# Kernel optimization log

Measured on AMD Instinct MI355X. Metric: run time of the kernel, lower is better.

The kernel has to match this reference:

```python
import jax, jax.numpy as jnp
import numpy as np

GAMMA = 0.997
N_STEPS = 5
EPS = 1e-3
Q_WEIGHTS = np.array([1.0, 0.5, 0.0, 2.0], dtype=np.float32)


def _rescale(x):
    # sign(x) * (sqrt(|x|+1) - 1) + eps * x
    return jnp.sign(x) * (jnp.sqrt(jnp.abs(x) + 1.0) - 1.0) + EPS * x


def _inv_rescale(x):
    sign = jnp.sign(x)
    sqrt_arg = 1.0 + 4.0 * EPS * (jnp.abs(x) + 1.0 + EPS)
    square = ((jnp.sqrt(sqrt_arg) - 1.0) / (2.0 * EPS)) ** 2
    return sign * (square - 1.0)


def setup_inputs() -> dict:
    key = jax.random.key(0)
    ks = jax.random.split(key, 6)
    B, T, Q = 4096, 512, 4
    current_q_value = jax.random.normal(ks[0], (B, T, Q), dtype=jnp.float32)
    next_q_value = jax.random.normal(ks[1], (B, T, Q), dtype=jnp.float32)
    log_p = jax.random.normal(ks[2], (B, T), dtype=jnp.float32)
    reward = jax.random.normal(ks[3], (B, T, Q), dtype=jnp.float32)
    is_done = jax.random.bernoulli(ks[4], 0.02, (B, T)).astype(jnp.float32)
    mask = jax.random.bernoulli(ks[5], 0.95, (B, T)).astype(jnp.float32)
    return {
        "current_q_value": current_q_value,
        "next_q_value": next_q_value,
        "log_p": log_p,
        "reward": reward,
        "is_done": is_done,
        "mask": mask,
    }


def reference(current_q_value, next_q_value, log_p, reward, is_done, mask):
    B, T, Q = reward.shape
    q_w = jnp.asarray(Q_WEIGHTS)[None, None, :]                     # (1,1,Q)
    nz = (q_w != 0)
    inv_qw = jnp.where(nz, 1.0 / jnp.where(nz, q_w, 1.0), 0.0)      # (1,1,Q)
    inv_num_q = 1.0 / float((Q_WEIGHTS != 0).sum())

    m = mask[..., None]                                             # (B,T,1)
    d = is_done[..., None]                                          # (B,T,1)

    nq = m * (1.0 - d) * _inv_rescale(next_q_value)                 # (B,T,Q)
    lp = inv_num_q * inv_qw * (m * (1.0 - d) * log_p[..., None])    # (B,T,Q)

    pad = jnp.zeros((B, N_STEPS - 1, Q), dtype=reward.dtype)
    pad_reward = jnp.concatenate([m * reward, pad], axis=1)         # (B,T+n-1,Q)
    lp_pad = jnp.concatenate([lp, pad], axis=1)                     # (B,T+n-1,Q)

    gpow = GAMMA ** jnp.arange(N_STEPS, dtype=jnp.float32)          # gamma^0..gamma^{n-1}
    widx = jnp.arange(T)[:, None] + jnp.arange(N_STEPS)[None, :]    # (T,n) window indices

    reward_sum = jnp.einsum('btnq,n->btq', pad_reward[:, widx, :], gpow)
    log_p_sum = jnp.einsum('btnq,n->btq', lp_pad[:, widx, :], gpow * GAMMA)

    idxs = jnp.minimum(T - 1, jnp.arange(T) + N_STEPS - 1)          # (T,)
    # NOTE: original code uses gamma**idx (absolute index), reproduced faithfully
    next_term = (GAMMA ** idxs.astype(jnp.float32))[None, :, None] * nq[:, idxs, :]

    target = _rescale(reward_sum + next_term + log_p_sum)           # (B,T,Q)
    loss = 0.5 * m * q_w * (current_q_value - target) ** 2
    return loss
```

## Files before the change

### kernel.cpp

```cpp
#include <hip/hip_runtime.h>
#include <math.h>

#define T_DIM 512
#define GAMMA_F 0.997f
#define EPS_F 1e-3f
#define LOG2_GAMMA (-0.0043345907f)

typedef float v4f __attribute__((ext_vector_type(4)));

__device__ __forceinline__ float inv_rescale_f(float x) {
    float s = (x > 0.f) ? 1.f : ((x < 0.f) ? -1.f : 0.f);
    float sqrt_arg = 1.f + 4.f * EPS_F * (fabsf(x) + 1.f + EPS_F);
    float q = (sqrtf(sqrt_arg) - 1.f) * (1.f / (2.f * EPS_F));
    return s * (q * q - 1.f);
}

__device__ __forceinline__ float rescale_f(float x) {
    return copysignf(sqrtf(fabsf(x) + 1.f) - 1.f, x) + EPS_F * x;
}

__global__ __launch_bounds__(512) void nstep_qloss_kernel(
    const float* __restrict__ cur_q,
    const float* __restrict__ next_q,
    const float* __restrict__ log_p,
    const float* __restrict__ reward,
    const float* __restrict__ is_done,
    const float* __restrict__ mask,
    float* __restrict__ out)
{
    __shared__ v4f   s_mr [T_DIM + 4];
    __shared__ float s_lpv[T_DIM + 4];
    __shared__ float s_md [T_DIM + 4];

    const int t    = threadIdx.x;
    const int base = blockIdx.x * T_DIM;
    const int idx  = base + t;
    const int s4   = (t + 4 < T_DIM) ? t + 4 : T_DIM - 1;

    const v4f* rew4 = (const v4f*)reward;
    const v4f* nq4  = (const v4f*)next_q;
    const v4f* cq4  = (const v4f*)cur_q;
    v4f*       out4 = (v4f*)out;

    float m = mask[idx];
    float d = is_done[idx];
    float p = log_p[idx];
    v4f   r = rew4[idx];
    v4f  nq = nq4[base + s4];
    v4f  cq = cq4[idx];

    float md = m * (1.f - d);
    s_mr [t] = m * r;
    s_lpv[t] = md * p;
    s_md [t] = md;
    if (t == T_DIM - 1) {
        v4f z; z.x = 0.f; z.y = 0.f; z.z = 0.f; z.w = 0.f;
        #pragma unroll
        for (int k = 1; k <= 4; ++k) {
            s_mr [T_DIM - 1 + k] = z;
            s_lpv[T_DIM - 1 + k] = 0.f;
            s_md [T_DIM - 1 + k] = md;
        }
    }
    __syncthreads();

    const float g1 = GAMMA_F;
    const float g2 = g1 * g1;
    const float g3 = g2 * g1;
    const float g4 = g2 * g2;

    v4f A0 = s_mr[t];
    v4f A1 = s_mr[t + 1];
    v4f A2 = s_mr[t + 2];
    v4f A3 = s_mr[t + 3];
    v4f A4 = s_mr[t + 4];
    float l0 = s_lpv[t];
    float l1 = s_lpv[t + 1];
    float l2 = s_lpv[t + 2];
    float l3 = s_lpv[t + 3];
    float l4 = s_lpv[t + 4];
    float md4 = s_md[t + 4];

    float a0 = A0.x, a1 = A0.y, a3 = A0.w;
    a0 = fmaf(g1, A1.x, a0); a1 = fmaf(g1, A1.y, a1); a3 = fmaf(g1, A1.w, a3);
    a0 = fmaf(g2, A2.x, a0); a1 = fmaf(g2, A2.y, a1); a3 = fmaf(g2, A2.w, a3);
    a0 = fmaf(g3, A3.x, a0); a1 = fmaf(g3, A3.y, a1); a3 = fmaf(g3, A3.w, a3);
    a0 = fmaf(g4, A4.x, a0); a1 = fmaf(g4, A4.y, a1); a3 = fmaf(g4, A4.w, a3);

    float Ls = l0;
    Ls = fmaf(g1, l1, Ls);
    Ls = fmaf(g2, l2, Ls);
    Ls = fmaf(g3, l3, Ls);
    Ls = fmaf(g4, l4, Ls);
    Ls *= GAMMA_F * (1.f / 3.f);

    float coeff = exp2f((float)s4 * LOG2_GAMMA);
    float g = coeff * md4;
    float nt0 = g * inv_rescale_f(nq.x);
    float nt1 = g * inv_rescale_f(nq.y);
    float nt3 = g * inv_rescale_f(nq.w);

    float tgt0 = rescale_f(a0 + nt0 + 1.0f * Ls);
    float tgt1 = rescale_f(a1 + nt1 + 2.0f * Ls);
    float tgt3 = rescale_f(a3 + nt3 + 0.5f * Ls);

    float hm = 0.5f * m;
    float e0 = cq.x - tgt0;
    float e1 = cq.y - tgt1;
    float e3 = cq.w - tgt3;
    v4f o;
    o.x = hm * e0 * e0;
    o.y = hm * 0.5f * e1 * e1;
    o.z = 0.f;
    o.w = hm * 2.0f * e3 * e3;
    out4[idx] = o;
}

extern "C" void kernel_launch(void* const* d_in, const int* in_sizes, int n_in,
                              void* d_out, int out_size, void* d_ws, size_t ws_size,
                              hipStream_t stream) {
    const float* cur_q   = (const float*)d_in[0];
    const float* next_q  = (const float*)d_in[1];
    const float* log_p   = (const float*)d_in[2];
    const float* reward  = (const float*)d_in[3];
    const float* is_done = (const float*)d_in[4];
    const float* mask    = (const float*)d_in[5];
    float* out = (float*)d_out;

    int BT = in_sizes[2];
    int blocks = BT / T_DIM;
    hipLaunchKernelGGL(nstep_qloss_kernel, dim3(blocks), dim3(512), 0, stream,
                       cur_q, next_q, log_p, reward, is_done, mask, out);
}
```

Before: 159.6 us.

## Make kernel persistent with double-buffered shared memory and next-row prefetch

Launches a capped grid of blocks that loop over rows with a grid stride, double-buffering the shared-memory staging arrays. The next row's global loads are issued before the barrier so they overlap the current row's computation. Per-thread constants are hoisted out of the loop. This is meant to hide memory latency and amortize launch/block overhead, at the cost of fewer resident blocks and higher register pressure.

New measurement: 162.7 us. No clear change (+2.0%).

```diff
diff --git a/kernel.cpp b/kernel.cpp
--- a/kernel.cpp
+++ b/kernel.cpp
@@ -26,94 +26,126 @@
     const float* __restrict__ reward,
     const float* __restrict__ is_done,
     const float* __restrict__ mask,
-    float* __restrict__ out)
+    float* __restrict__ out,
+    int nrows)
 {
-    __shared__ v4f   s_mr [T_DIM + 4];
-    __shared__ float s_lpv[T_DIM + 4];
-    __shared__ float s_md [T_DIM + 4];
+    __shared__ v4f   s_mr [2][T_DIM + 4];
+    __shared__ float s_lpv[2][T_DIM + 4];
+    __shared__ float s_md [2][T_DIM + 4];
 
-    const int t    = threadIdx.x;
-    const int base = blockIdx.x * T_DIM;
-    const int idx  = base + t;
-    const int s4   = (t + 4 < T_DIM) ? t + 4 : T_DIM - 1;
+    const int t  = threadIdx.x;
+    const int s4 = (t + 4 < T_DIM) ? t + 4 : T_DIM - 1;
+    const float coeff = exp2f((float)s4 * LOG2_GAMMA);
+
+    const float g1 = GAMMA_F;
+    const float g2 = g1 * g1;
+    const float g3 = g2 * g1;
+    const float g4 = g2 * g2;
+    const float LSC = GAMMA_F * (1.f / 3.f);
 
     const v4f* rew4 = (const v4f*)reward;
     const v4f* nq4  = (const v4f*)next_q;
     const v4f* cq4  = (const v4f*)cur_q;
     v4f*       out4 = (v4f*)out;
 
-    float m = mask[idx];
-    float d = is_done[idx];
-    float p = log_p[idx];
-    v4f   r = rew4[idx];
+    int row = blockIdx.x;
+    const int rstride = gridDim.x;
+    if (row >= nrows) return;
+
+    int base = row * T_DIM;
+    float m = mask[base + t];
+    float d = is_done[base + t];
+    float p = log_p[base + t];
+    v4f   r = rew4[base + t];
     v4f  nq = nq4[base + s4];
-    v4f  cq = cq4[idx];
+    v4f  cq = cq4[base + t];
 
-    float md = m * (1.f - d);
-    s_mr [t] = m * r;
-    s_lpv[t] = md * p;
-    s_md [t] = md;
-    if (t == T_DIM - 1) {
-        v4f z; z.x = 0.f; z.y = 0.f; z.z = 0.f; z.w = 0.f;
-        #pragma unroll
-        for (int k = 1; k <= 4; ++k) {
-            s_mr [T_DIM - 1 + k] = z;
-            s_lpv[T_DIM - 1 + k] = 0.f;
-            s_md [T_DIM - 1 + k] = md;
+    int k = 0;
+    for (;;) {
+        const int cur = k & 1;
+        const int obase = base;
+
+        const float m_c  = m;
+        const v4f   nq_c = nq;
+        const v4f   cq_c = cq;
+
+        float md = m * (1.f - d);
+        s_mr [cur][t] = m * r;
+        s_lpv[cur][t] = md * p;
+        s_md [cur][t] = md;
+        if (t == T_DIM - 1) {
+            v4f z; z.x = 0.f; z.y = 0.f; z.z = 0.f; z.w = 0.f;
+            #pragma unroll
+            for (int j = 1; j <= 4; ++j) {
+                s_mr [cur][T_DIM - 1 + j] = z;
+                s_lpv[cur][T_DIM - 1 + j] = 0.f;
+                s_md [cur][T_DIM - 1 + j] = md;
+            }
         }
+
+        const int nrow = row + rstride;
+        const bool more = (nrow < nrows);
+        if (more) {
+            base = nrow * T_DIM;
+            m  = mask[base + t];
+            d  = is_done[base + t];
+            p  = log_p[base + t];
+            r  = rew4[base + t];
+            nq = nq4[base + s4];
+            cq = cq4[base + t];
+        }
+
+        __syncthreads();
+
+        v4f A0 = s_mr[cur][t];
+        v4f A1 = s_mr[cur][t + 1];
+        v4f A2 = s_mr[cur][t + 2];
+        v4f A3 = s_mr[cur][t + 3];
+        v4f A4 = s_mr[cur][t + 4];
+        float l0 = s_lpv[cur][t];
+        float l1 = s_lpv[cur][t + 1];
+        float l2 = s_lpv[cur][t + 2];
+        float l3 = s_lpv[cur][t + 3];
+        float l4 = s_lpv[cur][t + 4];
+        float md4 = s_md[cur][t + 4];
+
+        float a0 = A0.x, a1 = A0.y, a3 = A0.w;
+        a0 = fmaf(g1, A1.x, a0); a1 = fmaf(g1, A1.y, a1); a3 = fmaf(g1, A1.w, a3);
+        a0 = fmaf(g2, A2.x, a0); a1 = fmaf(g2, A2.y, a1); a3 = fmaf(g2, A2.w, a3);
+        a0 = fmaf(g3, A3.x, a0); a1 = fmaf(g3, A3.y, a1); a3 = fmaf(g3, A3.w, a3);
+        a0 = fmaf(g4, A4.x, a0); a1 = fmaf(g4, A4.y, a1); a3 = fmaf(g4, A4.w, a3);
+
+        float Ls = l0;
+        Ls = fmaf(g1, l1, Ls);
+        Ls = fmaf(g2, l2, Ls);
+        Ls = fmaf(g3, l3, Ls);
+        Ls = fmaf(g4, l4, Ls);
+        Ls *= LSC;
+
+        float g = coeff * md4;
+        float nt0 = g * inv_rescale_f(nq_c.x);
+        float nt1 = g * inv_rescale_f(nq_c.y);
+        float nt3 = g * inv_rescale_f(nq_c.w);
+
+        float tgt0 = rescale_f(a0 + nt0 + 1.0f * Ls);
+        float tgt1 = rescale_f(a1 + nt1 + 2.0f * Ls);
+        float tgt3 = rescale_f(a3 + nt3 + 0.5f * Ls);
+
+        float hm = 0.5f * m_c;
+        float e0 = cq_c.x - tgt0;
+        float e1 = cq_c.y - tgt1;
+        float e3 = cq_c.w - tgt3;
+        v4f o;
+        o.x = hm * e0 * e0;
+        o.y = hm * 0.5f * e1 * e1;
+        o.z = 0.f;
+        o.w = hm * 2.0f * e3 * e3;
+        out4[obase + t] = o;
+
+        if (!more) break;
+        row = nrow;
+        ++k;
     }
-    __syncthreads();
-
-    const float g1 = GAMMA_F;
-    const float g2 = g1 * g1;
-    const float g3 = g2 * g1;
-    const float g4 = g2 * g2;
-
-    v4f A0 = s_mr[t];
-    v4f A1 = s_mr[t + 1];
-    v4f A2 = s_mr[t + 2];
-    v4f A3 = s_mr[t + 3];
-    v4f A4 = s_mr[t + 4];
-    float l0 = s_lpv[t];
-    float l1 = s_lpv[t + 1];
-    float l2 = s_lpv[t + 2];
-    float l3 = s_lpv[t + 3];
-    float l4 = s_lpv[t + 4];
-    float md4 = s_md[t + 4];
-
-    float a0 = A0.x, a1 = A0.y, a3 = A0.w;
-    a0 = fmaf(g1, A1.x, a0); a1 = fmaf(g1, A1.y, a1); a3 = fmaf(g1, A1.w, a3);
-    a0 = fmaf(g2, A2.x, a0); a1 = fmaf(g2, A2.y, a1); a3 = fmaf(g2, A2.w, a3);
-    a0 = fmaf(g3, A3.x, a0); a1 = fmaf(g3, A3.y, a1); a3 = fmaf(g3, A3.w, a3);
-    a0 = fmaf(g4, A4.x, a0); a1 = fmaf(g4, A4.y, a1); a3 = fmaf(g4, A4.w, a3);
-
-    float Ls = l0;
-    Ls = fmaf(g1, l1, Ls);
-    Ls = fmaf(g2, l2, Ls);
-    Ls = fmaf(g3, l3, Ls);
-    Ls = fmaf(g4, l4, Ls);
-    Ls *= GAMMA_F * (1.f / 3.f);
-
-    float coeff = exp2f((float)s4 * LOG2_GAMMA);
-    float g = coeff * md4;
-    float nt0 = g * inv_rescale_f(nq.x);
-    float nt1 = g * inv_rescale_f(nq.y);
-    float nt3 = g * inv_rescale_f(nq.w);
-
-    float tgt0 = rescale_f(a0 + nt0 + 1.0f * Ls);
-    float tgt1 = rescale_f(a1 + nt1 + 2.0f * Ls);
-    float tgt3 = rescale_f(a3 + nt3 + 0.5f * Ls);
-
-    float hm = 0.5f * m;
-    float e0 = cq.x - tgt0;
-    float e1 = cq.y - tgt1;
-    float e3 = cq.w - tgt3;
-    v4f o;
-    o.x = hm * e0 * e0;
-    o.y = hm * 0.5f * e1 * e1;
-    o.z = 0.f;
-    o.w = hm * 2.0f * e3 * e3;
-    out4[idx] = o;
 }
 
 extern "C" void kernel_launch(void* const* d_in, const int* in_sizes, int n_in,
@@ -128,7 +160,8 @@
     float* out = (float*)d_out;
 
     int BT = in_sizes[2];
-    int blocks = BT / T_DIM;
+    int nrows = BT / T_DIM;
+    int blocks = (nrows < 1024) ? nrows : 1024;
     hipLaunchKernelGGL(nstep_qloss_kernel, dim3(blocks), dim3(512), 0, stream,
-                       cur_q, next_q, log_p, reward, is_done, mask, out);
+                       cur_q, next_q, log_p, reward, is_done, mask, out, nrows);
 }
```
